# Kernel optimization log

Measured on AMD Instinct MI355X. Metric: run time of the kernel, lower is better.

Reference implementation:

```python
import jax, jax.numpy as jnp
import numpy as np
from jax import lax

HEAD = 8; DIM = 16; R = 3; R_T = 2
K_AREA = (2 * R + 1) ** 2   # 49 window positions
NT = 2 * R_T + 1            # 5 time taps
POSENC_SCALE = 10; N_FREQ = 10  # enc_dims=64 -> 64//(2*3)=10 freqs per axis


def conv3d(x, w, b):
    y = lax.conv_general_dilated(x, w, (1, 1, 1), 'SAME',
                                 dimension_numbers=('NCDHW', 'OIDHW', 'NCDHW'))
    return y + b[None, :, None, None, None]


def make_coord2(h, w):
    # LIIF-style pixel-center coords in [-1,1], channel order (y, x)
    ys = -1.0 + (2.0 * jnp.arange(h) + 1.0) / h
    xs = -1.0 + (2.0 * jnp.arange(w) + 1.0) / w
    yy, xx = jnp.meshgrid(ys, xs, indexing='ij')
    return jnp.stack([yy, xx], -1)


def gather2d_nearest(img, coord_yx):
    # img (B,C,H,W); coord (B,Q,K,2) normalized (y,x); grid_sample nearest, align_corners=False, zero pad
    B, C, H, W = img.shape
    iy = jnp.round(((coord_yx[..., 0] + 1.0) * H - 1.0) / 2.0)
    ix = jnp.round(((coord_yx[..., 1] + 1.0) * W - 1.0) / 2.0)
    valid = (iy >= 0) & (iy < H) & (ix >= 0) & (ix < W)
    idx = (jnp.clip(iy, 0, H - 1) * W + jnp.clip(ix, 0, W - 1)).astype(jnp.int32)
    flat = idx.reshape(B, -1)
    out = jnp.take_along_axis(img.reshape(B, C, H * W), flat[:, None, :], axis=2)
    out = out.reshape(B, C, *idx.shape[1:]) * valid[:, None].astype(img.dtype)
    return out  # (B,C,Q,K)


def trilinear(vol, coord_tyx):
    # vol (B,C,D,H,W); coord (B,Q,3) normalized (t,y,x); grid_sample bilinear 3D, align_corners=False, zero pad
    B, C, D, H, W = vol.shape
    iz = ((coord_tyx[..., 0] + 1.0) * D - 1.0) / 2.0
    iy = ((coord_tyx[..., 1] + 1.0) * H - 1.0) / 2.0
    ix = ((coord_tyx[..., 2] + 1.0) * W - 1.0) / 2.0
    z0 = jnp.floor(iz); y0 = jnp.floor(iy); x0 = jnp.floor(ix)
    wz = iz - z0; wy = iy - y0; wx = ix - x0
    volf = vol.reshape(B, C, D * H * W)

    def corner(zc, yc, xc, w):
        valid = (zc >= 0) & (zc < D) & (yc >= 0) & (yc < H) & (xc >= 0) & (xc < W)
        idx = (jnp.clip(zc, 0, D - 1) * (H * W) + jnp.clip(yc, 0, H - 1) * W
               + jnp.clip(xc, 0, W - 1)).astype(jnp.int32)
        v = jnp.take_along_axis(volf, idx[:, None, :], axis=2)  # (B,C,Q)
        return v * (w * valid.astype(vol.dtype))[:, None, :]

    out = 0.0
    for dz in (0, 1):
        for dy in (0, 1):
            for dx in (0, 1):
                w = ((wz if dz else 1 - wz) * (wy if dy else 1 - wy)
                     * (wx if dx else 1 - wx))
                out = out + corner(z0 + dz, y0 + dy, x0 + dx, w)
    return out  # (B,C,Q)


def forward(feat_img, scale, times, W_ch, b_ch, W_q, b_q, W_k, b_k, W_v, b_v,
            B_pe, W_pb, b_pb, W1, b1, W2, b2, W3, b3, W4, b4, W5, b5):
    feat = conv3d(feat_img, W_ch, b_ch)
    bs, fc, ft, fh, fw = feat.shape
    times_np = np.asarray(times).reshape(-1) * (ft - 1)
    Hh, Wh = fh * scale, fw * scale
    hr = make_coord2(Hh, Wh).reshape(1, -1, 2).astype(feat.dtype)
    hr = jnp.broadcast_to(hr, (bs, Hh * Wh, 2))  # (B,Q,2)
    q = hr.shape[1]
    # nearest LR pixel-center coords (grid_sample nearest over coord map)
    iy = jnp.clip(jnp.round(((hr[..., 0] + 1) * fh - 1) / 2), 0, fh - 1)
    ix = jnp.clip(jnp.round(((hr[..., 1] + 1) * fw - 1) / 2), 0, fw - 1)
    center = jnp.stack([-1 + (2 * iy + 1) / fh, -1 + (2 * ix + 1) / fw], -1)[:, :, None, :]
    dh = jnp.linspace(-R, R, 2 * R + 1) * (2.0 / fh)
    dw = jnp.linspace(-R, R, 2 * R + 1) * (2.0 / fw)
    gy, gx = jnp.meshgrid(dh, dw, indexing='ij')
    delta = jnp.stack([gy, gx], -1).reshape(1, 1, -1, 2)
    samp_k = center + delta  # (B,Q,K,2) key sampling coords
    feat_q = conv3d(feat, W_q, b_q)
    feat_k = conv3d(feat, W_k, b_k)
    feat_v = conv3d(feat, W_v, b_v)
    rel_cell = jnp.full((bs, q, 2), 2.0 / scale, feat.dtype)
    rel0 = hr[:, :, None, :] - samp_k  # (B,Q,K,2)
    dhd = DIM // HEAD
    preds = []
    for t in times_np:
        ct = int(round(float(t)))
        rel_time = (float(t) - ct) * 2.0 / NT
        idxs = np.clip(ct + np.arange(-R_T, R_T + 1), 0, ft - 1)
        fq_w = feat_q[:, :, idxs]
        fk_w = feat_k[:, :, idxs]
        fv_w = feat_v[:, :, idxs]
        coord3d = jnp.concatenate([jnp.full_like(hr[..., :1], rel_time), hr], -1)
        sq = trilinear(fq_w, coord3d)  # (B,C,Q)
        qh = sq.transpose(0, 2, 1).reshape(bs, q, HEAD, dhd)
        feats = []
        for dt in range(NT):
            tc = rel_time - (dt - R_T) * 2.0 / NT
            rel = jnp.concatenate([jnp.full_like(rel0[..., :1], tc), rel0], -1)
            rel = rel * jnp.asarray([NT, fh, fw], rel.dtype)
            proj = rel @ B_pe.T  # (B,Q,K,3*N_FREQ)
            enc = jnp.concatenate([jnp.sin(proj), jnp.cos(proj)], -1)
            pb = enc @ W_pb + b_pb  # (B,Q,K,HEAD), gamma=1
            kf = gather2d_nearest(fk_w[:, :, dt], samp_k).transpose(0, 2, 3, 1)
            kf = kf.reshape(bs, q, K_AREA, HEAD, dhd)
            scores = jnp.einsum('bqhd,bqkhd->bqkh', qh, kf) / np.sqrt(dhd).astype(np.float32)
            attn = jax.nn.softmax(scores + pb, axis=2)  # softmax over window
            vf = gather2d_nearest(fv_w[:, :, dt], samp_k).transpose(0, 2, 3, 1)
            vf = vf.reshape(bs, q, K_AREA, HEAD, dhd)
            feats.append((vf * attn[..., None]).reshape(bs, q, -1))
        feat_in = jnp.concatenate(feats, -1)           # (B,Q,DIM*K_AREA*NT)
        feat_back = sq.transpose(0, 2, 1)              # (B,Q,DIM)
        feat_in = jnp.concatenate([feat_in, feat_back, rel_cell], -1)
        h = jax.nn.gelu(feat_in @ W1 + b1, approximate=False)
        h = jax.nn.gelu(h @ W2 + b2, approximate=False)
        h = jax.nn.gelu(h @ W3 + b3, approximate=False)
        h = jax.nn.gelu(h @ W4 + b4, approximate=False)
        pred = (h @ W5 + b5).transpose(0, 2, 1).reshape(bs, 3, Hh, Wh)
        preds.append(pred)
    return jnp.stack(preds, 0)  # (n_times, B, 3, Hh, Wh)


def setup_inputs() -> dict:
    key = jax.random.key(0)
    ks = jax.random.split(key, 24)
    bs, in_dim, T, fh, fw = 1, 64, 6, 32, 32
    dim, head = 16, 8
    mlp_in = dim * K_AREA * NT + dim + 2  # 3938

    def w(k, shape, s=0.02):
        return jax.random.normal(k, shape, jnp.float32) * s

    freqs = 2.0 ** np.linspace(0, POSENC_SCALE, N_FREQ)
    B_pe = np.zeros((3 * N_FREQ, 3), np.float32)
    for a in range(3):
        B_pe[a * N_FREQ:(a + 1) * N_FREQ, a] = freqs
    return {
        'feat_img': jax.random.normal(ks[0], (bs, in_dim, T, fh, fw), jnp.float32),
        'scale': 4,
        'times': jax.random.uniform(ks[1], (1,), jnp.float32),
        'W_ch': w(ks[2], (dim, in_dim, 3, 3, 3)), 'b_ch': w(ks[3], (dim,)),
        'W_q': w(ks[4], (dim, dim, 3, 3, 3)), 'b_q': w(ks[5], (dim,)),
        'W_k': w(ks[6], (dim, dim, 3, 3, 3)), 'b_k': w(ks[7], (dim,)),
        'W_v': w(ks[8], (dim, dim, 3, 3, 3)), 'b_v': w(ks[9], (dim,)),
        'B_pe': jnp.asarray(B_pe),
        'W_pb': w(ks[10], (2 * 3 * N_FREQ, head)), 'b_pb': w(ks[11], (head,)),
        'W1': w(ks[12], (mlp_in, 256)), 'b1': w(ks[13], (256,)),
        'W2': w(ks[14], (256, 256)), 'b2': w(ks[15], (256,)),
        'W3': w(ks[16], (256, 256)), 'b3': w(ks[17], (256,)),
        'W4': w(ks[18], (256, 256)), 'b4': w(ks[19], (256,)),
        'W5': w(ks[20], (256, 3)), 'b5': w(ks[21], (3,)),
    }


def reference(feat_img, scale, times, W_ch, b_ch, W_q, b_q, W_k, b_k, W_v, b_v,
              B_pe, W_pb, b_pb, W1, b1, W2, b2, W3, b3, W4, b4, W5, b5):
    return forward(feat_img, scale, times, W_ch, b_ch, W_q, b_q, W_k, b_k, W_v, b_v,
                   B_pe, W_pb, b_pb, W1, b1, W2, b2, W3, b3, W4, b4, W5, b5)
```

## Files before the change

### kernel.cpp

```cpp
#include <hip/hip_runtime.h>

typedef __attribute__((ext_vector_type(8))) short bf16x8;
typedef __attribute__((ext_vector_type(8))) unsigned short u16x8;
typedef __attribute__((ext_vector_type(4))) float f32x4;

#define WSB_FEAT 0u
#define WSB_FQ   393216u
#define WSB_FK   786432u
#define WSB_FV   1179648u
#define WSB_META 1572864u
#define WSB_HA0  1574912u
#define WSB_HA1  18352128u
#define WSB_W1H  35129344u
#define WSB_W234 39258112u
#define WSB_FEAT1 39651328u

#define NH 256

__device__ __forceinline__ float gelu_f(float x) {
  return 0.5f * x * (1.0f + erff(x * 0.70710678118654752f));
}
__device__ __forceinline__ unsigned short f2bf(float x) {
  unsigned int u = __float_as_uint(x);
  u += 0x7fffu + ((u >> 16) & 1u);
  return (unsigned short)(u >> 16);
}
__device__ __forceinline__ float bf2f(unsigned short h) {
  return __uint_as_float(((unsigned int)h) << 16);
}
__device__ __forceinline__ void split2(float a, unsigned short& hi, unsigned short& lo) {
  hi = f2bf(a);
  lo = f2bf(a - bf2f(hi));
}
__device__ __forceinline__ unsigned int cvt_pk_bf16(float a, float b) {
  unsigned int r;
  asm("v_cvt_pk_bf16_f32 %0, %1, %2" : "=v"(r) : "v"(a), "v"(b));
  return r;
}

__global__ __launch_bounds__(512) void pre_kernel(
    const float* __restrict__ in, const float* __restrict__ W,
    const float* __restrict__ times, const float* __restrict__ Bpe,
    const float* __restrict__ Wpb, const float* __restrict__ bpb,
    const float* __restrict__ W1, const float* __restrict__ W2,
    const float* __restrict__ W3, const float* __restrict__ W4,
    float* __restrict__ feat0, float* __restrict__ feat1,
    float* __restrict__ meta,
    unsigned short* __restrict__ W1h, unsigned short* __restrict__ W234h) {
  __shared__ float win[4896];
  const int tid = threadIdx.x;
  if (blockIdx.x < 384) {
    const int half = blockIdx.x / 192;
    const int sp = blockIdx.x - half*192;
    const int t = sp >> 5, y = sp & 31;
    const int x = tid & 31, cop = tid >> 5;
    float acc = 0.f;
    const int cbase = half*32;
    for (int ci0 = cbase; ci0 < cbase + 32; ci0 += 16) {
      __syncthreads();
      for (int e = tid; e < 4896; e += 512) {
        int ci = e / 306, rem = e - ci*306;
        int tz = rem / 102, rem2 = rem - tz*102;
        int dy = rem2 / 34, xx = rem2 - dy*34;
        int gt = t + tz - 1, gy = y + dy - 1, gx = xx - 1;
        float v = 0.f;
        if (gt >= 0 && gt < 6 && gy >= 0 && gy < 32 && gx >= 0 && gx < 32)
          v = in[((ci0 + ci)*6 + gt)*1024 + gy*32 + gx];
        win[e] = v;
      }
      __syncthreads();
      for (int ci = 0; ci < 16; ++ci) {
        const float* w0 = W + (cop*64 + ci0 + ci)*27;
        const float* wr = win + ci*306;
        #pragma unroll
        for (int tz = 0; tz < 3; ++tz)
          #pragma unroll
          for (int dy = 0; dy < 3; ++dy)
            #pragma unroll
            for (int dx = 0; dx < 3; ++dx)
              acc += wr[(tz*3 + dy)*34 + x + dx] * w0[(tz*3 + dy)*3 + dx];
      }
    }
    float* dst = half ? feat1 : feat0;
    dst[(t*1024 + y*32 + x)*16 + cop] = acc;
  } else if (blockIdx.x == 384) {
    const float t5f = times[0] * 5.0f;
    const double ct_d = rint((double)t5f);
    const int ct = (int)ct_d;
    const double rt = ((double)t5f - ct_d) * 2.0 / 5.0;
    const float rtf = (float)rt;
    if (tid == 0) {
      float iz = ((rtf + 1.0f)*5.0f - 1.0f) / 2.0f;
      float z0 = floorf(iz);
      meta[0] = iz - z0;
      meta[1] = z0;
      for (int d = 0; d < 5; ++d) {
        int ix = ct + d - 2; ix = ix < 0 ? 0 : (ix > 5 ? 5 : ix);
        meta[2 + d] = (float)ix;
      }
    }
    if (tid < 40) {
      int dt = tid >> 3, h = tid & 7;
      double tcd = rt - (double)(dt - 2) * 2.0 / 5.0;
      float rs = (float)tcd * 5.0f;
      float acc = bpb[h];
      for (int j = 0; j < 10; ++j) {
        float pr = rs * Bpe[j*3 + 0];
        acc += sinf(pr) * Wpb[j*8 + h] + cosf(pr) * Wpb[(30+j)*8 + h];
      }
      meta[16 + tid] = acc;
    }
    if (tid < 224) {
      int p = tid / 56, ky = (tid >> 3) % 7, h = tid & 7;
      float r = (float)(2*p - 3) * 0.25f - 2.0f * (float)(ky - 3);
      float accy = 0.f, accx = 0.f;
      for (int j = 0; j < 10; ++j) {
        float pry = r * Bpe[(10+j)*3 + 1];
        accy += sinf(pry) * Wpb[(10+j)*8 + h] + cosf(pry) * Wpb[(40+j)*8 + h];
        float prx = r * Bpe[(20+j)*3 + 2];
        accx += sinf(prx) * Wpb[(20+j)*8 + h] + cosf(prx) * Wpb[(50+j)*8 + h];
      }
      meta[64 + tid]  = accy;
      meta[288 + tid] = accx;
    }
  } else if (tid < 256) {
    const int rblk = blockIdx.x - 385;
    const int n = tid;
    unsigned short tmp[32];
    if (rblk < 126) {
      const int s = rblk;
      #pragma unroll
      for (int j = 0; j < 32; ++j) {
        int p = s*32 + j;
        float w = 0.f;
        if (p < 4000) {
          int dt = p / 800, r = p - dt*800;
          if (r < 784) w = W1[(dt*784 + r)*256 + n];
        } else {
          int j2 = p - 4000;
          if (j2 < 18) w = W1[(3920 + j2)*256 + n];
        }
        tmp[j] = f2bf(w);
      }
      unsigned short* dh = W1h + ((size_t)(s*256 + n))*32;
      #pragma unroll
      for (int v = 0; v < 4; ++v) {
        u16x8 xv;
        #pragma unroll
        for (int j = 0; j < 8; ++j) xv[j] = tmp[v*8 + j];
        *(u16x8*)(dh + v*8) = xv;
      }
    } else {
      const int blk = rblk - 126;
      const int m = blk >> 3, s = blk & 7;
      const float* Wm = (m == 0) ? W2 : ((m == 1) ? W3 : W4);
      #pragma unroll
      for (int j = 0; j < 32; ++j) tmp[j] = f2bf(Wm[(s*32 + j)*256 + n]);
      unsigned short* dh = W234h + (size_t)m*65536 + ((size_t)(s*256 + n))*32;
      #pragma unroll
      for (int v = 0; v < 4; ++v) {
        u16x8 xv;
        #pragma unroll
        for (int j = 0; j < 8; ++j) xv[j] = tmp[v*8 + j];
        *(u16x8*)(dh + v*8) = xv;
      }
    }
  }
}

__global__ __launch_bounds__(512) void conv_qkv_kernel(
    const float* __restrict__ f0, const float* __restrict__ f1,
    const float* __restrict__ bch,
    const float* __restrict__ Wq, const float* __restrict__ bq,
    const float* __restrict__ Wk, const float* __restrict__ bk,
    const float* __restrict__ Wv, const float* __restrict__ bv,
    float* __restrict__ fq, float* __restrict__ fk, float* __restrict__ fv) {
  __shared__ float win[4896];
  __shared__ float sbch[16];
  const int blk = blockIdx.x;
  const int m = blk / 192;
  const int sp = blk - m*192;
  const int t = sp >> 5, y = sp & 31;
  const int tid = threadIdx.x;
  const int x = tid & 31, cop = tid >> 5;
  if (tid < 16) sbch[tid] = bch[tid];
  __syncthreads();
  for (int e = tid; e < 4896; e += 512) {
    int tz = e / 1632, rem = e - tz*1632;
    int dy = rem / 544, rem2 = rem - dy*544;
    int ci = rem2 / 34, xx = rem2 - ci*34;
    int gt = t + tz - 1, gy = y + dy - 1, gx = xx - 1;
    float v = 0.f;
    if (gt >= 0 && gt < 6 && gy >= 0 && gy < 32 && gx >= 0 && gx < 32) {
      const int idx = ((gt*32 + gy)*32 + gx)*16 + ci;
      v = f0[idx] + f1[idx] + sbch[ci];
    }
    win[e] = v;
  }
  __syncthreads();
  const float* Wm = (m == 0) ? Wq : ((m == 1) ? Wk : Wv);
  const float* bm = (m == 0) ? bq : ((m == 1) ? bk : bv);
  float*       fm = (m == 0) ? fq : ((m == 1) ? fk : fv);
  float a0 = 0.f, a1 = 0.f;
  for (int ci = 0; ci < 16; ci += 2) {
    const float* w0 = Wm + (cop*16 + ci)*27;
    #pragma unroll
    for (int tz = 0; tz < 3; ++tz)
      #pragma unroll
      for (int dy = 0; dy < 3; ++dy) {
        const float* wr0 = win + ((tz*3 + dy)*16 + ci)*34 + x;
        #pragma unroll
        for (int dx = 0; dx < 3; ++dx) {
          const int tap = (tz*3 + dy)*3 + dx;
          a0 += wr0[dx]      * w0[tap];
          a1 += wr0[34 + dx] * w0[27 + tap];
        }
      }
  }
  fm[(t*1024 + y*32 + x)*16 + cop] = a0 + a1 + bm[cop];
}

__device__ __forceinline__ void load_kv_regs(
    int tg, int cj0, int ci0, int tid,
    const float* __restrict__ fk, const float* __restrict__ fv,
    float (&kvr)[4]) {
  #pragma unroll
  for (int u = 0; u < 4; ++u) {
    const int e = tid + u*512;
    const int sel = e >> 10, r = e & 1023;
    const int wy8 = r >> 7, wx8 = (r >> 4) & 7, c = r & 15;
    const int gy = cj0 + wy8 - 3, gx = ci0 + wx8 - 3;
    float v = 0.f;
    if (gy >= 0 && gy < 32 && gx >= 0 && gx < 32)
      v = (sel ? fv : fk)[((tg*32 + gy)*32 + gx)*16 + c];
    kvr[u] = v;
  }
}

template<int CHL, int CHH, bool PRE>
__device__ __forceinline__ void attn_dt(
    int dt, int cj0, int ci0, int tid,
    int q, int h, int ay, int ax, int py, int px,
    int goct, int qr, int nb0,
    const float* __restrict__ fk, const float* __restrict__ fv,
    const unsigned short* __restrict__ W1h,
    const float* sPt, const float* sPy, const float* sPx,
    const float* sQh, float* sK, float* sV,
    unsigned short* sA0, unsigned short* sA1,
    float (&kvr)[4], int tg_next,
    f32x4 (&acc)[4][2]) {
  __syncthreads();
  #pragma unroll
  for (int u = 0; u < 4; ++u) {
    const int e = tid + u*512;
    const int sel = e >> 10, r = e & 1023;
    (sel ? sV : sK)[r] = kvr[u];
  }
  __syncthreads();

  const float qv0 = sQh[q*16 + 2*h], qv1 = sQh[q*16 + 2*h + 1];
  const float ptv = sPt[dt*8 + h];
  float ev[49];
  float ssum = 0.f;
  #pragma unroll
  for (int ky = 0; ky < 7; ++ky) {
    const float basey = ptv + sPy[(py*7 + ky)*8 + h];
    #pragma unroll
    for (int kx = 0; kx < 7; ++kx) {
      const float2 kv = *(const float2*)&sK[((ay + ky)*8 + ax + kx)*16 + 2*h];
      const float sc = (qv0*kv.x + qv1*kv.y) * 0.70710678118654752f + basey + sPx[(px*7 + kx)*8 + h];
      const float x = __expf(sc);
      ev[ky*7 + kx] = x;
      ssum += x;
    }
  }
  const float dinv = 1.f / ssum;

  if (PRE) load_kv_regs(tg_next, cj0, ci0, tid, fk, fv, kvr);

#define FILL_CHUNK(CH, BUF) do {                                            \
    _Pragma("unroll")                                                       \
    for (int kk = 0; kk < 10; ++kk) {                                       \
      const int k = (CH)*10 + kk;                                           \
      float a0 = 0.f, a1 = 0.f;                                             \
      if (k < 49) {                                                         \
        const int ky = k / 7, kx = k - ky*7;                                \
        const float e2 = ev[k] * dinv;                                      \
        const float2 vv = *(const float2*)&sV[((ay + ky)*8 + ax + kx)*16 + 2*h]; \
        a0 = e2 * vv.x; a1 = e2 * vv.y;                                     \
      }                                                                     \
      const int off = ((((kk >> 1)*4 + (kk & 1)*2 + (h >> 2))*4 + (q >> 4))*16 + (q & 15))*8 + 2*(h & 3); \
      *(unsigned int*)&(BUF)[off] = cvt_pk_bf16(a0, a1);                    \
    } } while (0)

  FILL_CHUNK(CHL, sA0);
  __syncthreads();
  #pragma unroll
  for (int ch = CHL; ch <= CHH; ++ch) {
    unsigned short* bufR = ((ch - CHL) & 1) ? sA1 : sA0;
    unsigned short* bufW = ((ch - CHL) & 1) ? sA0 : sA1;
    __builtin_amdgcn_s_setprio(1);
    #pragma unroll
    for (int sc2 = 0; sc2 < 5; ++sc2) {
      const int s_g = dt*25 + ch*5 + sc2;
      const unsigned short* bh_p = W1h + (size_t)(s_g*256 + nb0 + qr)*32 + goct*8;
      const bf16x8 bh0 = *(const bf16x8*)bh_p;
      const bf16x8 bh1 = *(const bf16x8*)(bh_p + 512);
      #pragma unroll
      for (int mt = 0; mt < 4; ++mt) {
        const int aoff = (((sc2*4 + goct)*4 + mt)*16 + qr)*8;
        const bf16x8 ah = *(const bf16x8*)&bufR[aoff];
        acc[mt][0] = __builtin_amdgcn_mfma_f32_16x16x32_bf16(ah, bh0, acc[mt][0], 0, 0, 0);
        acc[mt][1] = __builtin_amdgcn_mfma_f32_16x16x32_bf16(ah, bh1, acc[mt][1], 0, 0, 0);
      }
    }
    __builtin_amdgcn_s_setprio(0);
    if (ch < CHH) FILL_CHUNK(ch + 1, bufW);
    __syncthreads();
  }
#undef FILL_CHUNK
}

__global__ __launch_bounds__(512, 4) void attn_l1_kernel(
    const float* __restrict__ fq, const float* __restrict__ fk,
    const float* __restrict__ fv, const float* __restrict__ meta,
    const unsigned short* __restrict__ W1h,
    float* __restrict__ hA0, float* __restrict__ hA1) {
  __shared__ float sPt[40], sPy[224], sPx[224], sMeta[8];
  __shared__ float sQh[1024];
  __shared__ float sK[1024], sV[1024];
  __shared__ __align__(16) unsigned short sA0[10240];
  __shared__ __align__(16) unsigned short sA1[10240];

  const int tid = threadIdx.x;
  const int cp = blockIdx.x >> 1, bh = blockIdx.x & 1;
  const int cj0 = (cp >> 4) * 2, ci0 = (cp & 15) * 2;

  if (tid < 8) sMeta[tid] = meta[tid];
  if (tid < 40) sPt[tid] = meta[16 + tid];
  if (tid < 224) { sPy[tid] = meta[64 + tid]; sPx[tid] = meta[288 + tid]; }
  __syncthreads();
  const float wz = sMeta[0];
  const int z0 = (int)sMeta[1];
  const int tgz0 = (int)sMeta[2 + z0];
  const int tgz1 = (int)sMeta[3 + z0];
  const int tgd[5] = {(int)sMeta[2], (int)sMeta[3], (int)sMeta[4], (int)sMeta[5], (int)sMeta[6]};

  for (int e = tid; e < 1024; e += 512) {
    const int q = e >> 4, c = e & 15;
    const int pyp = q >> 3, pxp = q & 7;
    const int cj = cj0 + (pyp >> 2), ci = ci0 + (pxp >> 2);
    const int py = pyp & 3, px = pxp & 3;
    const int y0 = cj + ((py < 2) ? -1 : 0);
    const int x0 = ci + ((px < 2) ? -1 : 0);
    const float wy = (py == 0) ? 0.625f : (py == 1) ? 0.875f : (py == 2) ? 0.125f : 0.375f;
    const float wx = (px == 0) ? 0.625f : (px == 1) ? 0.875f : (px == 2) ? 0.125f : 0.375f;
    float s = 0.f;
    #pragma unroll
    for (int dz = 0; dz < 2; ++dz) {
      const int tg = dz ? tgz1 : tgz0;
      const float wzz = dz ? wz : (1.f - wz);
      #pragma unroll
      for (int dy = 0; dy < 2; ++dy) {
        const int yy = y0 + dy;
        const float wyy = dy ? wy : (1.f - wy);
        if (yy < 0 || yy > 31) continue;
        #pragma unroll
        for (int dx = 0; dx < 2; ++dx) {
          const int xx = x0 + dx;
          const float wxx = dx ? wx : (1.f - wx);
          if (xx < 0 || xx > 31) continue;
          s += ((wzz * wyy) * wxx) * fq[((tg*32 + yy)*32 + xx)*16 + c];
        }
      }
    }
    sQh[e] = s;
  }

  f32x4 acc[4][2];
  #pragma unroll
  for (int a = 0; a < 4; ++a) {
    acc[a][0] = (f32x4){0.f, 0.f, 0.f, 0.f};
    acc[a][1] = (f32x4){0.f, 0.f, 0.f, 0.f};
  }

  const int lane = tid & 63, wid = tid >> 6;
  const int goct = lane >> 4, qr = lane & 15;
  const int nb0 = wid * 32;
  const int q = tid >> 3, h = tid & 7;
  const int ay = q >> 5, ax = (q >> 2) & 1;
  const int py = (q >> 3) & 3, px = q & 3;

  float kvr[4];
  if (!bh) {
    load_kv_regs(tgd[0], cj0, ci0, tid, fk, fv, kvr);
    attn_dt<0,4,true >(0, cj0, ci0, tid, q, h, ay, ax, py, px, goct, qr, nb0,
                       fk, fv, W1h, sPt, sPy, sPx, sQh, sK, sV, sA0, sA1, kvr, tgd[1], acc);
    attn_dt<0,4,true >(1, cj0, ci0, tid, q, h, ay, ax, py, px, goct, qr, nb0,
                       fk, fv, W1h, sPt, sPy, sPx, sQh, sK, sV, sA0, sA1, kvr, tgd[2], acc);
    attn_dt<0,1,false>(2, cj0, ci0, tid, q, h, ay, ax, py, px, goct, qr, nb0,
                       fk, fv, W1h, sPt, sPy, sPx, sQh, sK, sV, sA0, sA1, kvr, 0, acc);
    __syncthreads();
    for (int e = tid; e < 2048; e += 512) {
      const int q2 = e >> 5, r2 = e & 31;
      const float a = (r2 < 16) ? sQh[q2*16 + r2] : ((r2 < 18) ? 0.5f : 0.f);
      const int off = ((((r2 >> 3))*4 + (q2 >> 4))*16 + (q2 & 15))*8 + (r2 & 7);
      sA0[off] = f2bf(a);
    }
    __syncthreads();
    const unsigned short* bh_p = W1h + (size_t)(125*256 + nb0 + qr)*32 + goct*8;
    const bf16x8 bh0 = *(const bf16x8*)bh_p;
    const bf16x8 bh1 = *(const bf16x8*)(bh_p + 512);
    #pragma unroll
    for (int mt = 0; mt < 4; ++mt) {
      const int aoff = ((goct*4 + mt)*16 + qr)*8;
      const bf16x8 ah = *(const bf16x8*)&sA0[aoff];
      acc[mt][0] = __builtin_amdgcn_mfma_f32_16x16x32_bf16(ah, bh0, acc[mt][0], 0, 0, 0);
      acc[mt][1] = __builtin_amdgcn_mfma_f32_16x16x32_bf16(ah, bh1, acc[mt][1], 0, 0, 0);
    }
  } else {
    load_kv_regs(tgd[2], cj0, ci0, tid, fk, fv, kvr);
    attn_dt<2,4,true >(2, cj0, ci0, tid, q, h, ay, ax, py, px, goct, qr, nb0,
                       fk, fv, W1h, sPt, sPy, sPx, sQh, sK, sV, sA0, sA1, kvr, tgd[3], acc);
    attn_dt<0,4,true >(3, cj0, ci0, tid, q, h, ay, ax, py, px, goct, qr, nb0,
                       fk, fv, W1h, sPt, sPy, sPx, sQh, sK, sV, sA0, sA1, kvr, tgd[4], acc);
    attn_dt<0,4,false>(4, cj0, ci0, tid, q, h, ay, ax, py, px, goct, qr, nb0,
                       fk, fv, W1h, sPt, sPy, sPx, sQh, sK, sV, sA0, sA1, kvr, 0, acc);
  }

  float* hp = bh ? hA1 : hA0;
  #pragma unroll
  for (int nt = 0; nt < 2; ++nt) {
    const int n = nb0 + nt*16 + qr;
    #pragma unroll
    for (int mt = 0; mt < 4; ++mt) {
      #pragma unroll
      for (int r = 0; r < 4; ++r) {
        const int ql = mt*16 + goct*4 + r;
        const int row = (cj0*4 + (ql >> 3))*128 + ci0*4 + (ql & 7);
        hp[row*NH + n] = acc[mt][nt][r];
      }
    }
  }
}

__global__ __launch_bounds__(512) void mlp234o_kernel(
    const float* __restrict__ hA0, const float* __restrict__ hA1,
    const unsigned short* __restrict__ W234h, const float* __restrict__ b1,
    const float* __restrict__ b2, const float* __restrict__ b3,
    const float* __restrict__ b4, const float* __restrict__ W5,
    const float* __restrict__ b5, float* __restrict__ out) {
  __shared__ __align__(16) unsigned short aH[8192];
  __shared__ __align__(16) unsigned short aL[8192];
  __shared__ float sW5[768];
  __shared__ float sB5[3];

  const int tid = threadIdx.x, lane = tid & 63, wid = tid >> 6;
  const int goct = lane >> 4, qr = lane & 15, nb0 = wid * 32;
  const int qbase = blockIdx.x * 32;

  for (int e = tid; e < 768; e += 512) sW5[e] = W5[e];
  if (tid < 3) sB5[tid] = b5[tid];

  {
    #pragma unroll
    for (int u = 0; u < 2; ++u) {
      const int idx = tid*2 + u;
      const int q0_ = idx >> 5, rem = idx & 31;
      const int s0_ = rem >> 2, g = rem & 3;
      const size_t off = (size_t)(qbase + q0_)*NH + s0_*32 + g*8;
      const float4 pa0 = *(const float4*)(hA0 + off);
      const float4 pa1 = *(const float4*)(hA0 + off + 4);
      const float4 pb0 = *(const float4*)(hA1 + off);
      const float4 pb1 = *(const float4*)(hA1 + off + 4);
      const float4 bb0 = *(const float4*)(b1 + s0_*32 + g*8);
      const float4 bb1 = *(const float4*)(b1 + s0_*32 + g*8 + 4);
      float vals[8] = {pa0.x + pb0.x + bb0.x, pa0.y + pb0.y + bb0.y,
                       pa0.z + pb0.z + bb0.z, pa0.w + pb0.w + bb0.w,
                       pa1.x + pb1.x + bb1.x, pa1.y + pb1.y + bb1.y,
                       pa1.z + pb1.z + bb1.z, pa1.w + pb1.w + bb1.w};
      bf16x8 hiv, lov;
      #pragma unroll
      for (int j = 0; j < 8; ++j) {
        const float v = gelu_f(vals[j]);
        unsigned short h_, l_;
        split2(v, h_, l_);
        hiv[j] = (short)h_; lov[j] = (short)l_;
      }
      const int ao = (((s0_*4 + g)*2 + (q0_ >> 4))*16 + (q0_ & 15))*8;
      *(bf16x8*)&aH[ao] = hiv;
      *(bf16x8*)&aL[ao] = lov;
    }
  }

  for (int layer = 0; layer < 3; ++layer) {
    const unsigned short* Wh = W234h + (size_t)layer*65536;
    const float* bptr = (layer == 0) ? b2 : ((layer == 1) ? b3 : b4);
    __syncthreads();
    f32x4 acc[2][2];
    #pragma unroll
    for (int a = 0; a < 2; ++a) {
      acc[a][0] = (f32x4){0.f, 0.f, 0.f, 0.f};
      acc[a][1] = (f32x4){0.f, 0.f, 0.f, 0.f};
    }
    #pragma unroll
    for (int s = 0; s < 8; ++s) {
      const unsigned short* bh_p = Wh + (size_t)(s*256 + nb0 + qr)*32 + goct*8;
      const bf16x8 bh0 = *(const bf16x8*)bh_p;
      const bf16x8 bh1 = *(const bf16x8*)(bh_p + 512);
      #pragma unroll
      for (int mt = 0; mt < 2; ++mt) {
        const int aoff = (((s*4 + goct)*2 + mt)*16 + qr)*8;
        const bf16x8 ah = *(const bf16x8*)&aH[aoff];
        const bf16x8 al = *(const bf16x8*)&aL[aoff];
        acc[mt][0] = __builtin_amdgcn_mfma_f32_16x16x32_bf16(ah, bh0, acc[mt][0], 0, 0, 0);
        acc[mt][0] = __builtin_amdgcn_mfma_f32_16x16x32_bf16(al, bh0, acc[mt][0], 0, 0, 0);
        acc[mt][1] = __builtin_amdgcn_mfma_f32_16x16x32_bf16(ah, bh1, acc[mt][1], 0, 0, 0);
        acc[mt][1] = __builtin_amdgcn_mfma_f32_16x16x32_bf16(al, bh1, acc[mt][1], 0, 0, 0);
      }
    }
    __syncthreads();
    #pragma unroll
    for (int nt = 0; nt < 2; ++nt) {
      const int n = nb0 + nt*16 + qr;
      const float bb = bptr[n];
      #pragma unroll
      for (int mt = 0; mt < 2; ++mt) {
        #pragma unroll
        for (int r = 0; r < 4; ++r) {
          const int qq = mt*16 + goct*4 + r;
          const float v = gelu_f(acc[mt][nt][r] + bb);
          unsigned short h_, l_; split2(v, h_, l_);
          const int ao = ((((n >> 5)*4 + ((n >> 3) & 3))*2 + mt)*16 + (qq & 15))*8 + (n & 7);
          aH[ao] = h_; aL[ao] = l_;
        }
      }
    }
  }
  __syncthreads();
  if (tid < 96) {
    const int c = tid >> 5, qq = tid & 31;
    const int mt = qq >> 4, qrr = qq & 15;
    float a = sB5[c];
    #pragma unroll 4
    for (int k8 = 0; k8 < 32; ++k8) {
      const int ao = ((k8*2 + mt)*16 + qrr)*8;
      const bf16x8 hv = *(const bf16x8*)&aH[ao];
      const bf16x8 lv = *(const bf16x8*)&aL[ao];
      #pragma unroll
      for (int j = 0; j < 8; ++j)
        a += (bf2f((unsigned short)hv[j]) + bf2f((unsigned short)lv[j])) * sW5[(k8*8 + j)*3 + c];
    }
    out[c*16384 + qbase + qq] = a;
  }
}

extern "C" void kernel_launch(void* const* d_in, const int* in_sizes, int n_in,
                              void* d_out, int out_size, void* d_ws, size_t ws_size,
                              hipStream_t stream) {
  const float* feat_img = (const float*)d_in[0];
  const float* times    = (const float*)d_in[2];
  const float* W_ch     = (const float*)d_in[3];
  const float* b_ch     = (const float*)d_in[4];
  const float* W_q      = (const float*)d_in[5];
  const float* b_q      = (const float*)d_in[6];
  const float* W_k      = (const float*)d_in[7];
  const float* b_k      = (const float*)d_in[8];
  const float* W_v      = (const float*)d_in[9];
  const float* b_v      = (const float*)d_in[10];
  const float* B_pe     = (const float*)d_in[11];
  const float* W_pb     = (const float*)d_in[12];
  const float* b_pb     = (const float*)d_in[13];
  const float* W1       = (const float*)d_in[14];
  const float* b1       = (const float*)d_in[15];
  const float* W2       = (const float*)d_in[16];
  const float* b2       = (const float*)d_in[17];
  const float* W3       = (const float*)d_in[18];
  const float* b3       = (const float*)d_in[19];
  const float* W4       = (const float*)d_in[20];
  const float* b4       = (const float*)d_in[21];
  const float* W5       = (const float*)d_in[22];
  const float* b5       = (const float*)d_in[23];

  char* wsb = (char*)d_ws;
  float* feat0 = (float*)(wsb + WSB_FEAT);
  float* feat1 = (float*)(wsb + WSB_FEAT1);
  float* fq   = (float*)(wsb + WSB_FQ);
  float* fk   = (float*)(wsb + WSB_FK);
  float* fv   = (float*)(wsb + WSB_FV);
  float* meta = (float*)(wsb + WSB_META);
  float* hA0  = (float*)(wsb + WSB_HA0);
  float* hA1  = (float*)(wsb + WSB_HA1);
  unsigned short* W1h   = (unsigned short*)(wsb + WSB_W1H);
  unsigned short* W234h = (unsigned short*)(wsb + WSB_W234);

  pre_kernel<<<535, 512, 0, stream>>>(feat_img, W_ch, times, B_pe, W_pb, b_pb,
                                      W1, W2, W3, W4, feat0, feat1, meta, W1h, W234h);
  conv_qkv_kernel<<<576, 512, 0, stream>>>(feat0, feat1, b_ch,
                                           W_q, b_q, W_k, b_k, W_v, b_v, fq, fk, fv);
  attn_l1_kernel<<<512, 512, 0, stream>>>(fq, fk, fv, meta, W1h, hA0, hA1);
  mlp234o_kernel<<<512, 512, 0, stream>>>(hA0, hA1, W234h, b1, b2, b3, b4, W5, b5, (float*)d_out);
}
```

Before: 169.0 us.

## Double-buffer K/V windows in LDS via async global_load_lds prefetch

The attention kernel now prefetches the next time step's K/V window straight into a second LDS buffer with global_load_lds, instead of staging it through registers and copying it into one shared buffer. Out-of-bounds taps read from a small zeroed workspace buffer, which pre_kernel initializes. This removes the two barriers and the register-to-LDS copy per time step and frees four registers per thread. It costs 8 KB more LDS and relies on the compiler placing correct vmcnt waits before the async-loaded data is read. The s_setprio hints around the MFMA loop are also dropped.

Measured after the change: 176.2 us. 1.04x slower.

```diff
diff --git a/kernel.cpp b/kernel.cpp
--- a/kernel.cpp
+++ b/kernel.cpp
@@ -12,6 +12,7 @@
 #define WSB_HA0  1574912u
 #define WSB_HA1  18352128u
 #define WSB_W1H  35129344u
+#define WSB_ZERO 37193728u
 #define WSB_W234 39258112u
 #define WSB_FEAT1 39651328u
 
@@ -36,6 +37,10 @@
   unsigned int r;
   asm("v_cvt_pk_bf16_f32 %0, %1, %2" : "=v"(r) : "v"(a), "v"(b));
   return r;
+}
+__device__ __forceinline__ void gload_lds4(const float* g, float* l) {
+  __builtin_amdgcn_global_load_lds((const __attribute__((address_space(1))) void*)g,
+                                   (__attribute__((address_space(3))) void*)l, 4, 0, 0);
 }
 
 __global__ __launch_bounds__(512) void pre_kernel(
@@ -45,7 +50,7 @@
     const float* __restrict__ W1, const float* __restrict__ W2,
     const float* __restrict__ W3, const float* __restrict__ W4,
     float* __restrict__ feat0, float* __restrict__ feat1,
-    float* __restrict__ meta,
+    float* __restrict__ meta, float* __restrict__ zbuf,
     unsigned short* __restrict__ W1h, unsigned short* __restrict__ W234h) {
   __shared__ float win[4896];
   const int tid = threadIdx.x;
@@ -84,6 +89,7 @@
     float* dst = half ? feat1 : feat0;
     dst[(t*1024 + y*32 + x)*16 + cop] = acc;
   } else if (blockIdx.x == 384) {
+    if (tid >= 64 && tid < 128) zbuf[tid - 64] = 0.f;
     const float t5f = times[0] * 5.0f;
     const double ct_d = rint((double)t5f);
     const int ct = (int)ct_d;
@@ -220,44 +226,37 @@
   fm[(t*1024 + y*32 + x)*16 + cop] = a0 + a1 + bm[cop];
 }
 
-__device__ __forceinline__ void load_kv_regs(
+__device__ __forceinline__ void issue_kv_async(
     int tg, int cj0, int ci0, int tid,
     const float* __restrict__ fk, const float* __restrict__ fv,
-    float (&kvr)[4]) {
+    const float* __restrict__ zbuf, float* sKn, float* sVn) {
   #pragma unroll
   for (int u = 0; u < 4; ++u) {
     const int e = tid + u*512;
     const int sel = e >> 10, r = e & 1023;
     const int wy8 = r >> 7, wx8 = (r >> 4) & 7, c = r & 15;
     const int gy = cj0 + wy8 - 3, gx = ci0 + wx8 - 3;
-    float v = 0.f;
-    if (gy >= 0 && gy < 32 && gx >= 0 && gx < 32)
-      v = (sel ? fv : fk)[((tg*32 + gy)*32 + gx)*16 + c];
-    kvr[u] = v;
+    const bool ok = (gy >= 0 && gy < 32 && gx >= 0 && gx < 32);
+    const float* src = ok ? ((sel ? fv : fk) + (((tg*32 + gy)*32 + gx)*16 + c))
+                          : (zbuf + c);
+    float* dstbase = (sel ? sVn : sKn) + (r & ~63);
+    gload_lds4(src, dstbase);
   }
 }
 
 template<int CHL, int CHH, bool PRE>
 __device__ __forceinline__ void attn_dt(
-    int dt, int cj0, int ci0, int tid,
+    int dt, int tg_next, int cj0, int ci0, int tid,
     int q, int h, int ay, int ax, int py, int px,
     int goct, int qr, int nb0,
     const float* __restrict__ fk, const float* __restrict__ fv,
+    const float* __restrict__ zbuf,
     const unsigned short* __restrict__ W1h,
     const float* sPt, const float* sPy, const float* sPx,
-    const float* sQh, float* sK, float* sV,
+    const float* sQh,
+    const float* sKc, const float* sVc, float* sKn, float* sVn,
     unsigned short* sA0, unsigned short* sA1,
-    float (&kvr)[4], int tg_next,
     f32x4 (&acc)[4][2]) {
-  __syncthreads();
-  #pragma unroll
-  for (int u = 0; u < 4; ++u) {
-    const int e = tid + u*512;
-    const int sel = e >> 10, r = e & 1023;
-    (sel ? sV : sK)[r] = kvr[u];
-  }
-  __syncthreads();
-
   const float qv0 = sQh[q*16 + 2*h], qv1 = sQh[q*16 + 2*h + 1];
   const float ptv = sPt[dt*8 + h];
   float ev[49];
@@ -267,7 +266,7 @@
     const float basey = ptv + sPy[(py*7 + ky)*8 + h];
     #pragma unroll
     for (int kx = 0; kx < 7; ++kx) {
-      const float2 kv = *(const float2*)&sK[((ay + ky)*8 + ax + kx)*16 + 2*h];
+      const float2 kv = *(const float2*)&sKc[((ay + ky)*8 + ax + kx)*16 + 2*h];
       const float sc = (qv0*kv.x + qv1*kv.y) * 0.70710678118654752f + basey + sPx[(px*7 + kx)*8 + h];
       const float x = __expf(sc);
       ev[ky*7 + kx] = x;
@@ -276,7 +275,7 @@
   }
   const float dinv = 1.f / ssum;
 
-  if (PRE) load_kv_regs(tg_next, cj0, ci0, tid, fk, fv, kvr);
+  if (PRE) issue_kv_async(tg_next, cj0, ci0, tid, fk, fv, zbuf, sKn, sVn);
 
 #define FILL_CHUNK(CH, BUF) do {                                            \
     _Pragma("unroll")                                                       \
@@ -286,7 +285,7 @@
       if (k < 49) {                                                         \
         const int ky = k / 7, kx = k - ky*7;                                \
         const float e2 = ev[k] * dinv;                                      \
-        const float2 vv = *(const float2*)&sV[((ay + ky)*8 + ax + kx)*16 + 2*h]; \
+        const float2 vv = *(const float2*)&sVc[((ay + ky)*8 + ax + kx)*16 + 2*h]; \
         a0 = e2 * vv.x; a1 = e2 * vv.y;                                     \
       }                                                                     \
       const int off = ((((kk >> 1)*4 + (kk & 1)*2 + (h >> 2))*4 + (q >> 4))*16 + (q & 15))*8 + 2*(h & 3); \
@@ -299,7 +298,6 @@
   for (int ch = CHL; ch <= CHH; ++ch) {
     unsigned short* bufR = ((ch - CHL) & 1) ? sA1 : sA0;
     unsigned short* bufW = ((ch - CHL) & 1) ? sA0 : sA1;
-    __builtin_amdgcn_s_setprio(1);
     #pragma unroll
     for (int sc2 = 0; sc2 < 5; ++sc2) {
       const int s_g = dt*25 + ch*5 + sc2;
@@ -314,7 +312,6 @@
         acc[mt][1] = __builtin_amdgcn_mfma_f32_16x16x32_bf16(ah, bh1, acc[mt][1], 0, 0, 0);
       }
     }
-    __builtin_amdgcn_s_setprio(0);
     if (ch < CHH) FILL_CHUNK(ch + 1, bufW);
     __syncthreads();
   }
@@ -324,11 +321,13 @@
 __global__ __launch_bounds__(512, 4) void attn_l1_kernel(
     const float* __restrict__ fq, const float* __restrict__ fk,
     const float* __restrict__ fv, const float* __restrict__ meta,
+    const float* __restrict__ zbuf,
     const unsigned short* __restrict__ W1h,
     float* __restrict__ hA0, float* __restrict__ hA1) {
   __shared__ float sPt[40], sPy[224], sPx[224], sMeta[8];
   __shared__ float sQh[1024];
-  __shared__ float sK[1024], sV[1024];
+  __shared__ float sK0[1024], sV0[1024];
+  __shared__ float sK1[1024], sV1[1024];
   __shared__ __align__(16) unsigned short sA0[10240];
   __shared__ __align__(16) unsigned short sA1[10240];
 
@@ -345,6 +344,8 @@
   const int tgz0 = (int)sMeta[2 + z0];
   const int tgz1 = (int)sMeta[3 + z0];
   const int tgd[5] = {(int)sMeta[2], (int)sMeta[3], (int)sMeta[4], (int)sMeta[5], (int)sMeta[6]};
+
+  issue_kv_async(bh ? tgd[2] : tgd[0], cj0, ci0, tid, fk, fv, zbuf, sK0, sV0);
 
   for (int e = tid; e < 1024; e += 512) {
     const int q = e >> 4, c = e & 15;
@@ -376,6 +377,7 @@
     }
     sQh[e] = s;
   }
+  __syncthreads();
 
   f32x4 acc[4][2];
   #pragma unroll
@@ -391,16 +393,13 @@
   const int ay = q >> 5, ax = (q >> 2) & 1;
   const int py = (q >> 3) & 3, px = q & 3;
 
-  float kvr[4];
   if (!bh) {
-    load_kv_regs(tgd[0], cj0, ci0, tid, fk, fv, kvr);
-    attn_dt<0,4,true >(0, cj0, ci0, tid, q, h, ay, ax, py, px, goct, qr, nb0,
-                       fk, fv, W1h, sPt, sPy, sPx, sQh, sK, sV, sA0, sA1, kvr, tgd[1], acc);
-    attn_dt<0,4,true >(1, cj0, ci0, tid, q, h, ay, ax, py, px, goct, qr, nb0,
-                       fk, fv, W1h, sPt, sPy, sPx, sQh, sK, sV, sA0, sA1, kvr, tgd[2], acc);
-    attn_dt<0,1,false>(2, cj0, ci0, tid, q, h, ay, ax, py, px, goct, qr, nb0,
-                       fk, fv, W1h, sPt, sPy, sPx, sQh, sK, sV, sA0, sA1, kvr, 0, acc);
-    __syncthreads();
+    attn_dt<0,4,true >(0, tgd[1], cj0, ci0, tid, q, h, ay, ax, py, px, goct, qr, nb0,
+                       fk, fv, zbuf, W1h, sPt, sPy, sPx, sQh, sK0, sV0, sK1, sV1, sA0, sA1, acc);
+    attn_dt<0,4,true >(1, tgd[2], cj0, ci0, tid, q, h, ay, ax, py, px, goct, qr, nb0,
+                       fk, fv, zbuf, W1h, sPt, sPy, sPx, sQh, sK1, sV1, sK0, sV0, sA0, sA1, acc);
+    attn_dt<0,1,false>(2, 0,      cj0, ci0, tid, q, h, ay, ax, py, px, goct, qr, nb0,
+                       fk, fv, zbuf, W1h, sPt, sPy, sPx, sQh, sK0, sV0, sK1, sV1, sA0, sA1, acc);
     for (int e = tid; e < 2048; e += 512) {
       const int q2 = e >> 5, r2 = e & 31;
       const float a = (r2 < 16) ? sQh[q2*16 + r2] : ((r2 < 18) ? 0.5f : 0.f);
@@ -419,13 +418,12 @@
       acc[mt][1] = __builtin_amdgcn_mfma_f32_16x16x32_bf16(ah, bh1, acc[mt][1], 0, 0, 0);
     }
   } else {
-    load_kv_regs(tgd[2], cj0, ci0, tid, fk, fv, kvr);
-    attn_dt<2,4,true >(2, cj0, ci0, tid, q, h, ay, ax, py, px, goct, qr, nb0,
-                       fk, fv, W1h, sPt, sPy, sPx, sQh, sK, sV, sA0, sA1, kvr, tgd[3], acc);
-    attn_dt<0,4,true >(3, cj0, ci0, tid, q, h, ay, ax, py, px, goct, qr, nb0,
-                       fk, fv, W1h, sPt, sPy, sPx, sQh, sK, sV, sA0, sA1, kvr, tgd[4], acc);
-    attn_dt<0,4,false>(4, cj0, ci0, tid, q, h, ay, ax, py, px, goct, qr, nb0,
-                       fk, fv, W1h, sPt, sPy, sPx, sQh, sK, sV, sA0, sA1, kvr, 0, acc);
+    attn_dt<2,4,true >(2, tgd[3], cj0, ci0, tid, q, h, ay, ax, py, px, goct, qr, nb0,
+                       fk, fv, zbuf, W1h, sPt, sPy, sPx, sQh, sK0, sV0, sK1, sV1, sA0, sA1, acc);
+    attn_dt<0,4,true >(3, tgd[4], cj0, ci0, tid, q, h, ay, ax, py, px, goct, qr, nb0,
+                       fk, fv, zbuf, W1h, sPt, sPy, sPx, sQh, sK1, sV1, sK0, sV0, sA0, sA1, acc);
+    attn_dt<0,4,false>(4, 0,      cj0, ci0, tid, q, h, ay, ax, py, px, goct, qr, nb0,
+                       fk, fv, zbuf, W1h, sPt, sPy, sPx, sQh, sK0, sV0, sK1, sV1, sA0, sA1, acc);
   }
 
   float* hp = bh ? hA1 : hA0;
@@ -589,15 +587,16 @@
   float* fk   = (float*)(wsb + WSB_FK);
   float* fv   = (float*)(wsb + WSB_FV);
   float* meta = (float*)(wsb + WSB_META);
+  float* zbuf = (float*)(wsb + WSB_ZERO);
   float* hA0  = (float*)(wsb + WSB_HA0);
   float* hA1  = (float*)(wsb + WSB_HA1);
   unsigned short* W1h   = (unsigned short*)(wsb + WSB_W1H);
   unsigned short* W234h = (unsigned short*)(wsb + WSB_W234);
 
   pre_kernel<<<535, 512, 0, stream>>>(feat_img, W_ch, times, B_pe, W_pb, b_pb,
-                                      W1, W2, W3, W4, feat0, feat1, meta, W1h, W234h);
+                                      W1, W2, W3, W4, feat0, feat1, meta, zbuf, W1h, W234h);
   conv_qkv_kernel<<<576, 512, 0, stream>>>(feat0, feat1, b_ch,
                                            W_q, b_q, W_k, b_k, W_v, b_v, fq, fk, fv);
-  attn_l1_kernel<<<512, 512, 0, stream>>>(fq, fk, fv, meta, W1h, hA0, hA1);
+  attn_l1_kernel<<<512, 512, 0, stream>>>(fq, fk, fv, meta, zbuf, W1h, hA0, hA1);
   mlp234o_kernel<<<512, 512, 0, stream>>>(hA0, hA1, W234h, b1, b2, b3, b4, W5, b5, (float*)d_out);
 }
```
